# Kernel tuning notes

Hardware: AMD Instinct MI355X
Metric: run time of the kernel (lower is better)

The kernel has to match this reference:

```python
import jax, jax.numpy as jnp
import numpy as np

B, T, C, H = 8, 1024, 768, 12
D = C // H  # head_dim = 64


def setup_inputs() -> dict:
    key = jax.random.key(0)
    ks = jax.random.split(key, 5)
    return {
        "x": jax.random.normal(ks[0], (B, T, C), dtype=jnp.float32),
        "W_in": jax.random.normal(ks[1], (C, 3 * C), dtype=jnp.float32) * 0.02,
        "b_in": jax.random.normal(ks[2], (3 * C,), dtype=jnp.float32) * 0.02,
        "W_out": jax.random.normal(ks[3], (C, C), dtype=jnp.float32) * 0.02,
        "b_out": jax.random.normal(ks[4], (C,), dtype=jnp.float32) * 0.02,
    }


def reference(x, W_in, b_in, W_out, b_out):
    b, t, c = x.shape
    qkv = x @ W_in + b_in                       # [b, t, 3c]
    # NOTE: original code splits as (k, q, v) -- k first!
    k, q, v = jnp.split(qkv, 3, axis=2)
    # [b, h, t, d]
    k = k.reshape(b, t, H, D).transpose(0, 2, 1, 3)
    q = q.reshape(b, t, H, D).transpose(0, 2, 1, 3)
    v = v.reshape(b, t, H, D).transpose(0, 2, 1, 3)
    # NOTE: original applies NO 1/sqrt(d) scaling.
    scores = jnp.einsum("bhqd,bhkd->bhqk", q, k)
    causal = jnp.tril(jnp.ones((t, t), dtype=bool))
    scores = jnp.where(causal[None, None], scores, -jnp.inf)
    attn = jax.nn.softmax(scores, axis=-1)
    y = jnp.einsum("bhqk,bhkd->bhqd", attn, v)  # [b, h, t, d]
    y = y.transpose(0, 2, 1, 3).reshape(b, t, c)
    return y @ W_out + b_out
```

## Files before the change

### kernel.cpp

```cpp
#include <hip/hip_runtime.h>
#include <hip/hip_bf16.h>
#include <stdint.h>


typedef __bf16 bf16;
typedef __attribute__((ext_vector_type(4))) __bf16 bf16x4;
typedef __attribute__((ext_vector_type(8))) __bf16 bf16x8;
typedef __attribute__((ext_vector_type(4))) float f32x4;

#define NB 8
#define NT 1024
#define NC 768
#define NH 12
#define ND 64
#define NM (NB*NT)
#define N3C (3*NC)

typedef __attribute__((address_space(1))) void as1_void;
typedef __attribute__((address_space(3))) void as3_void;

__device__ __forceinline__ void gload_lds16(const void* g, void* l) {
  __builtin_amdgcn_global_load_lds((as1_void*)g, (as3_void*)l, 16, 0, 0);
}


__global__ void k_convert(const float* __restrict__ src, bf16* __restrict__ dst, int n4) {
  int i = blockIdx.x * blockDim.x + threadIdx.x;
  if (i < n4) {
    float4 v = reinterpret_cast<const float4*>(src)[i];
    bf16x4 o = { (bf16)v.x, (bf16)v.y, (bf16)v.z, (bf16)v.w };
    reinterpret_cast<bf16x4*>(dst)[i] = o;
  }
}

__global__ void k_transpose_w(const float* __restrict__ src, bf16* __restrict__ dst,
                              int R, int C) {
  __shared__ float tile[32][33];
  const int c0 = blockIdx.x * 32, r0 = blockIdx.y * 32;
  const int tx = threadIdx.x & 31, ty = threadIdx.x >> 5;
#pragma unroll
  for (int i = 0; i < 4; i++)
    tile[ty + i*8][tx] = src[(size_t)(r0 + ty + i*8) * C + c0 + tx];
  __syncthreads();
#pragma unroll
  for (int i = 0; i < 4; i++)
    dst[(size_t)(c0 + ty + i*8) * R + r0 + tx] = (bf16)tile[tx][ty + i*8];
}

template<int MODE>
__global__ void k_gemm_bt(const bf16* __restrict__ A, const bf16* __restrict__ Bt,
                          const float* __restrict__ bias, float* __restrict__ Cout,
                          bf16* __restrict__ qp, bf16* __restrict__ kp,
                          bf16* __restrict__ vp,
                          int M, int N, int K) {
  __shared__ __align__(16) bf16 As[128*32];
  __shared__ __align__(16) bf16 Bs[128*32];
  const int tm = blockIdx.x * 128, tn = blockIdx.y * 128;
  const int tid = threadIdx.x, lane = tid & 63, w = tid >> 6;
  const int wr = w >> 1, wc = w & 1;
  const int lr = lane & 15, lhi = lane >> 4;
  const int srow = tid >> 2, scol = (tid & 3) * 8;

  f32x4 acc[4][4];
#pragma unroll
  for (int m = 0; m < 4; m++)
#pragma unroll
    for (int n = 0; n < 4; n++) acc[m][n] = (f32x4){0.f, 0.f, 0.f, 0.f};

  for (int kt = 0; kt < K; kt += 32) {
    __syncthreads();
#pragma unroll
    for (int ch = 0; ch < 2; ch++) {
      gload_lds16(A + (size_t)(tm + ch*64 + srow) * K + kt + scol,
                  (char*)As + ch*4096 + tid*16);
      gload_lds16(Bt + (size_t)(tn + ch*64 + srow) * K + kt + scol,
                  (char*)Bs + ch*4096 + tid*16);
    }
    __syncthreads();

    bf16x8 af[4], bfr[4];
#pragma unroll
    for (int m = 0; m < 4; m++)
      af[m] = *reinterpret_cast<const bf16x8*>(
          (const char*)As + (wr*64 + m*16 + lr) * 64 + lhi * 16);
#pragma unroll
    for (int n = 0; n < 4; n++)
      bfr[n] = *reinterpret_cast<const bf16x8*>(
          (const char*)Bs + (wc*64 + n*16 + lr) * 64 + lhi * 16);
#pragma unroll
    for (int m = 0; m < 4; m++)
#pragma unroll
      for (int n = 0; n < 4; n++)
        acc[m][n] = __builtin_amdgcn_mfma_f32_16x16x32_bf16(af[m], bfr[n], acc[m][n], 0, 0, 0);
  }

  if (MODE == 0) {
#pragma unroll
    for (int m = 0; m < 4; m++)
#pragma unroll
      for (int n = 0; n < 4; n++) {
        const int col = tn + wc*64 + n*16 + lr;
        const float bv = bias[col];
#pragma unroll
        for (int j = 0; j < 4; j++) {
          const int row = tm + wr*64 + m*16 + lhi*4 + j;
          Cout[(size_t)row * N + col] = acc[m][n][j] + bv;
        }
      }
  } else {
    const int part = tn / NC;
#pragma unroll
    for (int m = 0; m < 4; m++)
#pragma unroll
      for (int n = 0; n < 4; n++) {
        const int col = tn + wc*64 + n*16 + lr;
        const float bv = bias[col];
        const int cp = col - part * NC;
        const int h = cp >> 6, d = cp & 63;
#pragma unroll
        for (int j = 0; j < 4; j++) {
          const int row = tm + wr*64 + m*16 + lhi*4 + j;
          const int b0 = row >> 10, t = row & 1023;
          const int bh = b0 * NH + h;
          const bf16 val = (bf16)(acc[m][n][j] + bv);
          if (part == 2) {
            const size_t idx =
                ((((size_t)bh*16 + (t>>6))*4 + (d>>4))*2 + ((t>>5)&1))*512
                + (size_t)((d&15) + ((t>>3)&3)*16)*8 + (t&7);
            vp[idx] = val;
          } else {
            const size_t idx =
                (((size_t)bh*64 + (t>>4))*2 + (d>>5))*512
                + (size_t)(((d>>3)&3)*16 + (t&15))*8 + (d&7);
            if (part == 0) kp[idx] = val; else qp[idx] = val;
          }
        }
      }
  }
}

__global__ void __launch_bounds__(64, 2)
k_attn(const bf16* __restrict__ qpack, const bf16* __restrict__ kpack,
       const bf16* __restrict__ vpack, bf16* __restrict__ y) {
  const int bh = blockIdx.x, b = bh / NH, h = bh % NH;
  const int p = blockIdx.y;
  const int lane = threadIdx.x;
  const int lr = lane & 15, lhi = lane >> 4;
  __shared__ __align__(16) bf16 P[32][68];

#define LOAD_K(DST, K0)                                                        \
  {                                                                            \
    _Pragma("unroll")                                                          \
    for (int g = 0; g < 4; g++)                                                \
      _Pragma("unroll")                                                        \
      for (int h2 = 0; h2 < 2; h2++)                                           \
        DST[g][h2] = *reinterpret_cast<const bf16x8*>(                         \
            kpack + (((size_t)bh*64 + ((K0)>>4) + g)*2 + h2)*512 + lane*8);    \
  }

#define ATTN_STEP(KCUR, KNXT, KB)                                              \
  {                                                                            \
    const int k0 = (KB) * 64;                                                  \
    const int kn = ((KB) + 1 < nkb) ? k0 + 64 : k0;                            \
                        \
    bf16x8 vf[4][2];                                                           \
    _Pragma("unroll")                                                          \
    for (int dg = 0; dg < 4; dg++)                                             \
      _Pragma("unroll")                                                        \
      for (int kk = 0; kk < 2; kk++)                                           \
        vf[dg][kk] = *reinterpret_cast<const bf16x8*>(                         \
            vpack + ((((size_t)bh*16 + (k0>>6))*4 + dg)*2 + kk)*512 + lane*8); \
                   \
    LOAD_K(KNXT, kn);                                                          \
    f32x4 S[2][4];                                                             \
    _Pragma("unroll")                                                          \
    for (int m = 0; m < 2; m++)                                                \
      _Pragma("unroll")                                                        \
      for (int g = 0; g < 4; g++) S[m][g] = (f32x4){0.f, 0.f, 0.f, 0.f};       \
    _Pragma("unroll")                                                          \
    for (int g = 0; g < 4; g++)                                                \
      _Pragma("unroll")                                                        \
      for (int m = 0; m < 2; m++) {                                            \
        S[m][g] = __builtin_amdgcn_mfma_f32_16x16x32_bf16(qf[m][0], KCUR[g][0],\
                                                          S[m][g], 0, 0, 0);   \
        S[m][g] = __builtin_amdgcn_mfma_f32_16x16x32_bf16(qf[m][1], KCUR[g][1],\
                                                          S[m][g], 0, 0, 0);   \
      }                                                                        \
    const bool need_mask = ((KB) == nkb - 1);                                  \
    _Pragma("unroll")                                                          \
    for (int m = 0; m < 2; m++)                                                \
      _Pragma("unroll")                                                        \
      for (int g = 0; g < 4; g++) {                                            \
        const int key = k0 + g*16 + lr;                                        \
        _Pragma("unroll")                                                      \
        for (int j = 0; j < 4; j++) {                                          \
          float s = S[m][g][j];                                                \
          if (need_mask) {                                                     \
            const int row = qbase + m*16 + lhi*4 + j;                          \
            if (key > row) s = -1e30f;                                         \
          }                                                                    \
          const float ppv = __expf(s);   \
          L[m][j] += ppv;                                                      \
          P[m*16 + lhi*4 + j][g*16 + lr] = (bf16)ppv;                          \
        }                                                                      \
      }                                                                        \
    _Pragma("unroll")                                                          \
    for (int m = 0; m < 2; m++)                                                \
      _Pragma("unroll")                                                        \
      for (int kk = 0; kk < 2; kk++) {                                         \
        bf16x8 pf = *reinterpret_cast<const bf16x8*>(&P[m*16 + lr][kk*32 + lhi*8]); \
        _Pragma("unroll")                                                      \
        for (int dg = 0; dg < 4; dg++)                                         \
          O[m][dg] = __builtin_amdgcn_mfma_f32_16x16x32_bf16(pf, vf[dg][kk],   \
                                                             O[m][dg], 0, 0, 0); \
      }                                                                        \
  }

#pragma unroll 1
  for (int half = 0; half < 2; half++) {
    const int qt = half ? (31 - p) : p;
    const int qbase = qt * 32;
    const int nkb = (qbase >> 6) + 1;

    bf16x8 qf[2][2];
#pragma unroll
    for (int m = 0; m < 2; m++)
#pragma unroll
      for (int kk = 0; kk < 2; kk++)
        qf[m][kk] = *reinterpret_cast<const bf16x8*>(
            qpack + (((size_t)bh*64 + (qbase>>4) + m)*2 + kk)*512 + lane*8);

    f32x4 O[2][4];
    float L[2][4];
#pragma unroll
    for (int m = 0; m < 2; m++) {
#pragma unroll
      for (int d = 0; d < 4; d++) O[m][d] = (f32x4){0.f, 0.f, 0.f, 0.f};
#pragma unroll
      for (int j = 0; j < 4; j++) L[m][j] = 0.f;
    }

    bf16x8 kfA[4][2], kfB[4][2];
    LOAD_K(kfA, 0);
    int kb = 0;
#pragma unroll 1
    while (true) {
      ATTN_STEP(kfA, kfB, kb);
      kb++;
      if (kb >= nkb) break;
      ATTN_STEP(kfB, kfA, kb);
      kb++;
      if (kb >= nkb) break;
    }

#pragma unroll
    for (int m = 0; m < 2; m++)
#pragma unroll
      for (int j = 0; j < 4; j++) {
        float l = L[m][j];
        l += __shfl_xor(l, 1);
        l += __shfl_xor(l, 2);
        l += __shfl_xor(l, 4);
        l += __shfl_xor(l, 8);
        L[m][j] = 1.0f / l;
      }

#pragma unroll
    for (int m = 0; m < 2; m++)
#pragma unroll
      for (int dg = 0; dg < 4; dg++)
#pragma unroll
        for (int j = 0; j < 4; j++) {
          const int row = qbase + m*16 + lhi*4 + j;
          const int col = h*ND + dg*16 + lr;
          y[(size_t)(b*NT + row) * NC + col] = (bf16)(O[m][dg][j] * L[m][j]);
        }
  }
#undef ATTN_STEP
#undef LOAD_K
}

extern "C" void kernel_launch(void* const* d_in, const int* in_sizes, int n_in,
                              void* d_out, int out_size, void* d_ws, size_t ws_size,
                              hipStream_t stream) {
  const float* x     = (const float*)d_in[0];
  const float* W_in  = (const float*)d_in[1];
  const float* b_in  = (const float*)d_in[2];
  const float* W_out = (const float*)d_in[3];
  const float* b_out = (const float*)d_in[4];
  float* out = (float*)d_out;
  char* ws = (char*)d_ws;

  bf16* xb    = (bf16*)(ws + 0);
  bf16* Wit   = (bf16*)(ws + 12582912);
  bf16* Wot   = (bf16*)(ws + 16121856);
  bf16* qpack = (bf16*)(ws + 17301504);
  bf16* kpack = (bf16*)(ws + 29884416);
  bf16* vpack = (bf16*)(ws + 42467328);

  k_convert<<<6144, 256, 0, stream>>>(x, xb, NM * NC / 4);
  k_transpose_w<<<dim3(N3C/32, NC/32), 256, 0, stream>>>(W_in, Wit, NC, N3C);
  k_transpose_w<<<dim3(NC/32, NC/32), 256, 0, stream>>>(W_out, Wot, NC, NC);

  k_gemm_bt<1><<<dim3(NM/128, N3C/128), 256, 0, stream>>>(
      xb, Wit, b_in, nullptr, qpack, kpack, vpack, NM, N3C, NC);

  k_attn<<<dim3(NB*NH, 16), 64, 0, stream>>>(qpack, kpack, vpack, xb );

  k_gemm_bt<0><<<dim3(NM/128, NC/128), 256, 0, stream>>>(
      xb, Wot, b_out, out, nullptr, nullptr, nullptr, NM, NC, NC);
}
```

Measured before the change: 202.2 us.

## Triple-buffer GEMM LDS staging with async loads and XOR-swizzled tiles

```diff
diff --git a/kernel.cpp b/kernel.cpp
--- a/kernel.cpp
+++ b/kernel.cpp
@@ -48,51 +48,74 @@
 }
 
 template<int MODE>
-__global__ void k_gemm_bt(const bf16* __restrict__ A, const bf16* __restrict__ Bt,
-                          const float* __restrict__ bias, float* __restrict__ Cout,
-                          bf16* __restrict__ qp, bf16* __restrict__ kp,
-                          bf16* __restrict__ vp,
-                          int M, int N, int K) {
-  __shared__ __align__(16) bf16 As[128*32];
-  __shared__ __align__(16) bf16 Bs[128*32];
+__global__ void __launch_bounds__(256, 2)
+k_gemm_bt(const bf16* __restrict__ A, const bf16* __restrict__ Bt,
+          const float* __restrict__ bias, float* __restrict__ Cout,
+          bf16* __restrict__ qp, bf16* __restrict__ kp,
+          bf16* __restrict__ vp,
+          int M, int N, int K) {
+  __shared__ __align__(16) bf16 As[3][128*32];
+  __shared__ __align__(16) bf16 Bs[3][128*32];
   const int tm = blockIdx.x * 128, tn = blockIdx.y * 128;
   const int tid = threadIdx.x, lane = tid & 63, w = tid >> 6;
   const int wr = w >> 1, wc = w & 1;
   const int lr = lane & 15, lhi = lane >> 4;
-  const int srow = tid >> 2, scol = (tid & 3) * 8;
-
-  f32x4 acc[4][4];
-#pragma unroll
-  for (int m = 0; m < 4; m++)
-#pragma unroll
-    for (int n = 0; n < 4; n++) acc[m][n] = (f32x4){0.f, 0.f, 0.f, 0.f};
-
-  for (int kt = 0; kt < K; kt += 32) {
-    __syncthreads();
+  const int srow = tid >> 2;
+  const int scol = ((tid & 3) ^ ((tid >> 3) & 3)) * 8;
+  const int cswz = (lhi ^ ((lr >> 1) & 3)) * 16;
+  const int nk = K / 32;
+
+  auto stage = [&](bf16* as, bf16* bs, int kt) {
 #pragma unroll
     for (int ch = 0; ch < 2; ch++) {
       gload_lds16(A + (size_t)(tm + ch*64 + srow) * K + kt + scol,
-                  (char*)As + ch*4096 + tid*16);
+                  (char*)as + ch*4096 + tid*16);
       gload_lds16(Bt + (size_t)(tn + ch*64 + srow) * K + kt + scol,
-                  (char*)Bs + ch*4096 + tid*16);
+                  (char*)bs + ch*4096 + tid*16);
     }
-    __syncthreads();
+  };
+
+  f32x4 acc[4][4];
+#pragma unroll
+  for (int m = 0; m < 4; m++)
+#pragma unroll
+    for (int n = 0; n < 4; n++) acc[m][n] = (f32x4){0.f, 0.f, 0.f, 0.f};
+
+  bf16 *a0 = As[0], *a1 = As[1], *a2 = As[2];
+  bf16 *b0 = Bs[0], *b1 = Bs[1], *b2 = Bs[2];
+  stage(a0, b0, 0);
+  stage(a1, b1, 32);
+  asm volatile("s_waitcnt vmcnt(8)" ::: "memory");
+  __builtin_amdgcn_s_barrier();
+  __builtin_amdgcn_sched_barrier(0);
+
+  for (int t = 0; t < nk; ++t) {
+    const int ktn = (t + 2 < nk ? t + 2 : nk - 1) * 32;
+    stage(a2, b2, ktn);
 
     bf16x8 af[4], bfr[4];
 #pragma unroll
     for (int m = 0; m < 4; m++)
       af[m] = *reinterpret_cast<const bf16x8*>(
-          (const char*)As + (wr*64 + m*16 + lr) * 64 + lhi * 16);
+          (const char*)a0 + (wr*64 + m*16 + lr) * 64 + cswz);
 #pragma unroll
     for (int n = 0; n < 4; n++)
       bfr[n] = *reinterpret_cast<const bf16x8*>(
-          (const char*)Bs + (wc*64 + n*16 + lr) * 64 + lhi * 16);
+          (const char*)b0 + (wc*64 + n*16 + lr) * 64 + cswz);
 #pragma unroll
     for (int m = 0; m < 4; m++)
 #pragma unroll
       for (int n = 0; n < 4; n++)
         acc[m][n] = __builtin_amdgcn_mfma_f32_16x16x32_bf16(af[m], bfr[n], acc[m][n], 0, 0, 0);
-  }
+
+    asm volatile("s_waitcnt vmcnt(8)" ::: "memory");
+    __builtin_amdgcn_s_barrier();
+    __builtin_amdgcn_sched_barrier(0);
+
+    bf16* ra = a0; a0 = a1; a1 = a2; a2 = ra;
+    bf16* rb = b0; b0 = b1; b1 = b2; b2 = rb;
+  }
+  asm volatile("s_waitcnt vmcnt(0)" ::: "memory");
 
   if (MODE == 0) {
 #pragma unroll
@@ -120,8 +143,8 @@
 #pragma unroll
         for (int j = 0; j < 4; j++) {
           const int row = tm + wr*64 + m*16 + lhi*4 + j;
-          const int b0 = row >> 10, t = row & 1023;
-          const int bh = b0 * NH + h;
+          const int b0i = row >> 10, t = row & 1023;
+          const int bh = b0i * NH + h;
           const bf16 val = (bf16)(acc[m][n][j] + bv);
           if (part == 2) {
             const size_t idx =
```

New measurement: 200.7 us. About the same (-0.8%).
